# Optimization experiments

Measured on AMD Instinct MI355X. Metric: run time of the kernel, lower is better.

The kernel has to match this reference:

```python
import jax, jax.numpy as jnp
import numpy as np


def setup_inputs() -> dict:
    key = jax.random.key(0)
    k1, k2 = jax.random.split(key)
    B, C, H, W = 32, 8, 256, 256
    inp = jax.random.normal(k1, (B, C, H, W), dtype=jnp.float32)
    tgt = jax.random.uniform(k2, (B, C, H, W), dtype=jnp.float32)
    return {"input": inp, "target": tgt}


def reference(input, target):
    B, C, H, W = input.shape
    # normalized coordinate grids: (index+1)/size, as in the original loops
    x_grid = (jnp.arange(W, dtype=input.dtype) + 1.0) / W          # [W]
    y_grid = (jnp.arange(H, dtype=input.dtype) + 1.0) / H          # [H]

    # per-(b,c) softmax over the flattened heatmap (DSNT)
    p = jax.nn.softmax(input.reshape(B, C, H * W), axis=-1).reshape(B, C, H, W)
    pred_x = jnp.einsum('bchw,w->bc', p, x_grid)                   # [B, C]
    pred_y = jnp.einsum('bchw,h->bc', p, y_grid)                   # [B, C]

    # ground-truth coords from argmax of target heatmap
    idx = jnp.argmax(target.reshape(B, C, H * W), axis=-1)         # [B, C] int
    true_x = ((idx % W) + 1).astype(input.dtype) / W
    true_y = ((idx // W) + 1).astype(input.dtype) / H

    ed = jnp.sqrt((true_x - pred_x) ** 2 + (true_y - pred_y) ** 2)  # [B, C]
    # original sums over all (batch, channel) pairs, divides by batch size only
    return jnp.sum(ed) / B
```

## Files before the change

kernel.cpp:

```cpp
#include <hip/hip_runtime.h>
#include <math.h>


constexpr int HW    = 256 * 256;
constexpr int BLOCK = 1024;
constexpr int WAVES = BLOCK / 64;
constexpr int ITERS = (HW / 4) / BLOCK;

__global__ __launch_bounds__(BLOCK) void dsnt_loss_kernel(
        const float* __restrict__ input,
        const float* __restrict__ target,
        float* __restrict__ out)
{
    const int bc = blockIdx.x;
    const float4* __restrict__ in4 =
        reinterpret_cast<const float4*>(input) + (size_t)bc * (HW / 4);
    const float4* __restrict__ tg4 =
        reinterpret_cast<const float4*>(target) + (size_t)bc * (HW / 4);
    const int tid = threadIdx.x;

    float s = 0.f, sx = 0.f, sy = 0.f;
    float bv = -INFINITY;
    int   bi = 0x7FFFFFFF;

    #pragma unroll
    for (int i = 0; i < ITERS; ++i) {
        const int j = tid + i * BLOCK;
        const float4 v = in4[j];
        const float4 t = tg4[j];
        const int f = 4 * j;
        const float y  = (float)((f >> 8) + 1) * (1.0f / 256.0f);
        const float x0 = (float)((f & 255) + 1) * (1.0f / 256.0f);

        const float e0 = __expf(v.x);
        const float e1 = __expf(v.y);
        const float e2 = __expf(v.z);
        const float e3 = __expf(v.w);
        const float es = (e0 + e1) + (e2 + e3);
        s  += es;
        sy += es * y;
        sx += e0 * x0
            + e1 * (x0 + 1.0f / 256.0f)
            + e2 * (x0 + 2.0f / 256.0f)
            + e3 * (x0 + 3.0f / 256.0f);

        if (t.x > bv) { bv = t.x; bi = f; }
        if (t.y > bv) { bv = t.y; bi = f + 1; }
        if (t.z > bv) { bv = t.z; bi = f + 2; }
        if (t.w > bv) { bv = t.w; bi = f + 3; }
    }

    #pragma unroll
    for (int off = 32; off > 0; off >>= 1) {
        s  += __shfl_down(s, off);
        sx += __shfl_down(sx, off);
        sy += __shfl_down(sy, off);
        const float ov = __shfl_down(bv, off);
        const int   oi = __shfl_down(bi, off);
        if (ov > bv || (ov == bv && oi < bi)) { bv = ov; bi = oi; }
    }

    __shared__ float ls[WAVES], lsx[WAVES], lsy[WAVES], lbv[WAVES];
    __shared__ int   lbi[WAVES];
    const int wave = tid >> 6;
    const int lane = tid & 63;
    if (lane == 0) {
        ls[wave]  = s;
        lsx[wave] = sx;
        lsy[wave] = sy;
        lbv[wave] = bv;
        lbi[wave] = bi;
    }
    __syncthreads();

    if (tid == 0) {
        #pragma unroll
        for (int wv = 1; wv < WAVES; ++wv) {
            s  += ls[wv];
            sx += lsx[wv];
            sy += lsy[wv];
            if (lbv[wv] > bv || (lbv[wv] == bv && lbi[wv] < bi)) {
                bv = lbv[wv];
                bi = lbi[wv];
            }
        }
        const float px = sx / s;
        const float py = sy / s;
        const float tx = (float)((bi & 255) + 1) * (1.0f / 256.0f);
        const float ty = (float)((bi >> 8) + 1) * (1.0f / 256.0f);
        const float dx = tx - px;
        const float dy = ty - py;
        const float ed = sqrtf(dx * dx + dy * dy);
        atomicAdd(out, ed * (1.0f / 32.0f));
    }
}

extern "C" void kernel_launch(void* const* d_in, const int* in_sizes, int n_in,
                              void* d_out, int out_size, void* d_ws, size_t ws_size,
                              hipStream_t stream) {
    const float* input  = (const float*)d_in[0];
    const float* target = (const float*)d_in[1];
    float* out = (float*)d_out;

    const int n_maps = in_sizes[0] / HW;

    hipMemsetAsync(out, 0, sizeof(float), stream);
    dsnt_loss_kernel<<<n_maps, BLOCK, 0, stream>>>(input, target, out);
}
```

Before: 147.7 us.

## Split each heatmap across eight blocks and reduce in a second kernel

The single-block-per-map kernel becomes a partial kernel in which each of 256 maps is split into 8 chunks, for 2048 blocks of 256 threads. Per-chunk sums and a packed 64-bit argmax key go to workspace, and a one-block final kernel combines them and writes the loss. This replaces the memset and atomic and gives the GPU more blocks than the 256 it had, which were fewer than the MI355X has CUs. The cost is an extra kernel launch and a serial final reduction. The packed key assumes non-negative target values for the float-bits ordering.

```diff
diff --git a/kernel.cpp b/kernel.cpp
--- a/kernel.cpp
+++ b/kernel.cpp
@@ -3,32 +3,40 @@
 
 
 constexpr int HW    = 256 * 256;
-constexpr int BLOCK = 1024;
-constexpr int WAVES = BLOCK / 64;
-constexpr int ITERS = (HW / 4) / BLOCK;
+constexpr int BLOCK = 256;
+constexpr int SPLIT = 8;
+constexpr int CHUNK4 = (HW / 4) / SPLIT;
+constexpr int ITERS  = CHUNK4 / BLOCK;
 
-__global__ __launch_bounds__(BLOCK) void dsnt_loss_kernel(
+__global__ __launch_bounds__(BLOCK, 8) void dsnt_partial_kernel(
         const float* __restrict__ input,
         const float* __restrict__ target,
-        float* __restrict__ out)
+        unsigned long long* __restrict__ ws_pk,
+        float* __restrict__ ws_s,
+        float* __restrict__ ws_sx,
+        float* __restrict__ ws_sy)
 {
-    const int bc = blockIdx.x;
+    const int bc    = blockIdx.x >> 3;
+    const int chunk = blockIdx.x & (SPLIT - 1);
+    const int tid   = threadIdx.x;
+
     const float4* __restrict__ in4 =
-        reinterpret_cast<const float4*>(input) + (size_t)bc * (HW / 4);
+        reinterpret_cast<const float4*>(input) + (size_t)bc * (HW / 4) + chunk * CHUNK4;
     const float4* __restrict__ tg4 =
-        reinterpret_cast<const float4*>(target) + (size_t)bc * (HW / 4);
-    const int tid = threadIdx.x;
+        reinterpret_cast<const float4*>(target) + (size_t)bc * (HW / 4) + chunk * CHUNK4;
 
     float s = 0.f, sx = 0.f, sy = 0.f;
     float bv = -INFINITY;
     int   bi = 0x7FFFFFFF;
+
+    const int fbase = 4 * chunk * CHUNK4;
 
     #pragma unroll
     for (int i = 0; i < ITERS; ++i) {
         const int j = tid + i * BLOCK;
         const float4 v = in4[j];
         const float4 t = tg4[j];
-        const int f = 4 * j;
+        const int f = fbase + 4 * j;
         const float y  = (float)((f >> 8) + 1) * (1.0f / 256.0f);
         const float x0 = (float)((f & 255) + 1) * (1.0f / 256.0f);
 
@@ -50,48 +58,92 @@
         if (t.w > bv) { bv = t.w; bi = f + 3; }
     }
 
+    unsigned long long pk =
+        ((unsigned long long)__float_as_uint(bv) << 32) |
+        (unsigned long long)(0xFFFFFFFFu - (unsigned)bi);
+
     #pragma unroll
     for (int off = 32; off > 0; off >>= 1) {
         s  += __shfl_down(s, off);
         sx += __shfl_down(sx, off);
         sy += __shfl_down(sy, off);
-        const float ov = __shfl_down(bv, off);
-        const int   oi = __shfl_down(bi, off);
-        if (ov > bv || (ov == bv && oi < bi)) { bv = ov; bi = oi; }
+        const unsigned long long opk = __shfl_down(pk, off);
+        pk = (opk > pk) ? opk : pk;
     }
 
-    __shared__ float ls[WAVES], lsx[WAVES], lsy[WAVES], lbv[WAVES];
-    __shared__ int   lbi[WAVES];
+    __shared__ float ls[4], lsx[4], lsy[4];
+    __shared__ unsigned long long lpk[4];
     const int wave = tid >> 6;
     const int lane = tid & 63;
     if (lane == 0) {
         ls[wave]  = s;
         lsx[wave] = sx;
         lsy[wave] = sy;
-        lbv[wave] = bv;
-        lbi[wave] = bi;
+        lpk[wave] = pk;
     }
     __syncthreads();
 
     if (tid == 0) {
         #pragma unroll
-        for (int wv = 1; wv < WAVES; ++wv) {
+        for (int wv = 1; wv < 4; ++wv) {
             s  += ls[wv];
             sx += lsx[wv];
             sy += lsy[wv];
-            if (lbv[wv] > bv || (lbv[wv] == bv && lbi[wv] < bi)) {
-                bv = lbv[wv];
-                bi = lbi[wv];
-            }
+            pk = (lpk[wv] > pk) ? lpk[wv] : pk;
         }
+        const int slot = blockIdx.x;
+        ws_s[slot]  = s;
+        ws_sx[slot] = sx;
+        ws_sy[slot] = sy;
+        ws_pk[slot] = pk;
+    }
+}
+
+__global__ __launch_bounds__(256) void dsnt_final_kernel(
+        const unsigned long long* __restrict__ ws_pk,
+        const float* __restrict__ ws_s,
+        const float* __restrict__ ws_sx,
+        const float* __restrict__ ws_sy,
+        float* __restrict__ out,
+        int nmap)
+{
+    const int bc = threadIdx.x;
+    float ed = 0.f;
+    if (bc < nmap) {
+        float s = 0.f, sx = 0.f, sy = 0.f;
+        unsigned long long pk = 0ull;
+        #pragma unroll
+        for (int c = 0; c < SPLIT; ++c) {
+            const int slot = bc * SPLIT + c;
+            s  += ws_s[slot];
+            sx += ws_sx[slot];
+            sy += ws_sy[slot];
+            const unsigned long long p = ws_pk[slot];
+            pk = (p > pk) ? p : pk;
+        }
+        const unsigned bi = 0xFFFFFFFFu - (unsigned)(pk & 0xFFFFFFFFull);
         const float px = sx / s;
         const float py = sy / s;
         const float tx = (float)((bi & 255) + 1) * (1.0f / 256.0f);
         const float ty = (float)((bi >> 8) + 1) * (1.0f / 256.0f);
         const float dx = tx - px;
         const float dy = ty - py;
-        const float ed = sqrtf(dx * dx + dy * dy);
-        atomicAdd(out, ed * (1.0f / 32.0f));
+        ed = sqrtf(dx * dx + dy * dy);
+    }
+
+    #pragma unroll
+    for (int off = 32; off > 0; off >>= 1)
+        ed += __shfl_down(ed, off);
+
+    __shared__ float led[4];
+    const int wave = threadIdx.x >> 6;
+    const int lane = threadIdx.x & 63;
+    if (lane == 0) led[wave] = ed;
+    __syncthreads();
+
+    if (threadIdx.x == 0) {
+        const float total = (led[0] + led[1]) + (led[2] + led[3]);
+        out[0] = total * (1.0f / 32.0f);
     }
 }
 
@@ -103,7 +155,15 @@
     float* out = (float*)d_out;
 
     const int n_maps = in_sizes[0] / HW;
+    const int nslot  = n_maps * SPLIT;
 
-    hipMemsetAsync(out, 0, sizeof(float), stream);
-    dsnt_loss_kernel<<<n_maps, BLOCK, 0, stream>>>(input, target, out);
+    unsigned long long* ws_pk = (unsigned long long*)d_ws;
+    float* ws_s  = (float*)((char*)d_ws + (size_t)8  * nslot);
+    float* ws_sx = (float*)((char*)d_ws + (size_t)12 * nslot);
+    float* ws_sy = (float*)((char*)d_ws + (size_t)16 * nslot);
+
+    dsnt_partial_kernel<<<nslot, BLOCK, 0, stream>>>(input, target,
+                                                     ws_pk, ws_s, ws_sx, ws_sy);
+    dsnt_final_kernel<<<1, 256, 0, stream>>>(ws_pk, ws_s, ws_sx, ws_sy,
+                                             out, n_maps);
 }
```

After: 144.9 us. Within noise of the previous version (-1.9%).
